# Optimization experiments

Hardware: AMD Instinct MI355X
Metric: run time of the kernel (lower is better)

The kernel has to match this reference:

```python
import math
import jax, jax.numpy as jnp
import numpy as np

B, T, C = 4, 2048, 1024
NH = 16
HD = C // NH  # 64

def setup_inputs() -> dict:
    key = jax.random.key(0)
    k1, k2, k3 = jax.random.split(key, 3)
    x = jax.random.normal(k1, (B, T, C), dtype=jnp.float32)
    # init scale ~ 1/sqrt(fan_in) to keep activations sane
    W_attn = jax.random.normal(k2, (C, 3 * C), dtype=jnp.float32) * (1.0 / math.sqrt(C))
    b_attn = jnp.zeros((3 * C,), dtype=jnp.float32)
    W_proj = jax.random.normal(k3, (C, C), dtype=jnp.float32) * (1.0 / math.sqrt(C))
    b_proj = jnp.zeros((C,), dtype=jnp.float32)
    return {"x": x, "W_attn": W_attn, "b_attn": b_attn, "W_proj": W_proj, "b_proj": b_proj}

def reference(x, W_attn, b_attn, W_proj, b_proj):
    b, t, c = x.shape
    qkv = x @ W_attn + b_attn                      # [B,T,3C]
    q, k, v = jnp.split(qkv, 3, axis=-1)           # each [B,T,C]
    # [B,T,C] -> [B,NH,T,HD]
    def heads(z):
        return z.reshape(b, t, NH, HD).transpose(0, 2, 1, 3)
    q, k, v = heads(q), heads(k), heads(v)
    scale = 1.0 / math.sqrt(HD)
    att = jnp.einsum('bhqd,bhkd->bhqk', q, k) * scale   # [B,NH,T,T]
    causal = jnp.tril(jnp.ones((t, t), dtype=bool))      # [T,T]
    att = jnp.where(causal[None, None, :, :], att, -jnp.inf)
    att = jax.nn.softmax(att, axis=-1)
    # dropout p=0.0 -> identity
    y = jnp.einsum('bhqk,bhkd->bhqd', att, v)            # [B,NH,T,HD]
    y = y.transpose(0, 2, 1, 3).reshape(b, t, c)         # [B,T,C]
    return y @ W_proj + b_proj
```

## Files before the change

kernel.cpp:

```cpp
#include <hip/hip_runtime.h>
#include <hip/hip_bf16.h>


typedef __bf16 bf16;
typedef __bf16 bf16x4 __attribute__((ext_vector_type(4)));
typedef __bf16 bf16x8 __attribute__((ext_vector_type(8)));
typedef float  f32x4  __attribute__((ext_vector_type(4)));

#define MFMA16(a, b, c) __builtin_amdgcn_mfma_f32_16x16x32_bf16((a), (b), (c), 0, 0, 0)

#define GLOAD16(g, l)                                                 \
    __builtin_amdgcn_global_load_lds(                                 \
        (const __attribute__((address_space(1))) void*)(g),           \
        (__attribute__((address_space(3))) void*)(l), 16, 0, 0)

static constexpr int Bsz = 4;
static constexpr int T   = 2048;
static constexpr int Cc  = 1024;
static constexpr int NH  = 16;
static constexpr int HD  = 64;
static constexpr int C3  = 3 * Cc;

__global__ void cvt_f32_bf16(const float* __restrict__ in, bf16* __restrict__ out) {
    size_t i = ((size_t)blockIdx.x * blockDim.x + threadIdx.x) * 8;
    f32x4 a0 = *(const f32x4*)(in + i);
    f32x4 a1 = *(const f32x4*)(in + i + 4);
    bf16x8 v;
#pragma unroll
    for (int e = 0; e < 4; ++e) { v[e] = (bf16)a0[e]; v[e + 4] = (bf16)a1[e]; }
    *(bf16x8*)(out + i) = v;
}

__global__ void transpose_f32_bf16(const float* __restrict__ in, bf16* __restrict__ out,
                                   int R, int Ccols) {
    __shared__ float tile[32][33];
    int bx = blockIdx.x * 32;
    int by = blockIdx.y * 32;
    int tx = threadIdx.x, ty = threadIdx.y;
#pragma unroll
    for (int i = 0; i < 32; i += 8)
        tile[ty + i][tx] = in[(size_t)(by + ty + i) * Ccols + bx + tx];
    __syncthreads();
#pragma unroll
    for (int i = 0; i < 32; i += 8)
        out[(size_t)(bx + ty + i) * R + by + tx] = (bf16)tile[tx][ty + i];
}

__global__ __launch_bounds__(256)
void gemm_qkv(const bf16* __restrict__ A, const bf16* __restrict__ Bt,
              const float* __restrict__ bias,
              bf16* __restrict__ qo, bf16* __restrict__ ko, bf16* __restrict__ vt,
              int M, int N, int K) {
    constexpr int BM = 128, BN = 128, BK = 64;
    __shared__ bf16 As[2][BM * BK];
    __shared__ bf16 Bs[2][BN * BK];

    const int tid  = threadIdx.x;
    const int wave = tid >> 6, lane = tid & 63;
    const int quad = lane >> 4, l16 = lane & 15;
    const int wm = wave & 1, wn = wave >> 1;
    const int m0 = blockIdx.x * BM, n0 = blockIdx.y * BN;

    f32x4 acc[4][4] = {};

    const int lrow = lane >> 3;
    const int lcol = (lane & 7) * 8;
    const bf16* Ab = A  + (size_t)(m0 + wave * 8 + lrow) * K + lcol;
    const bf16* Bb = Bt + (size_t)(n0 + wave * 8 + lrow) * K + lcol;
    const int wofs = wave * 512;

#pragma unroll
    for (int r = 0; r < 4; ++r) {
        GLOAD16(Ab + (size_t)r * 32 * K, As[0] + wofs + r * 2048);
        GLOAD16(Bb + (size_t)r * 32 * K, Bs[0] + wofs + r * 2048);
    }

    int cur = 0;
    for (int k0 = 0; k0 < K; k0 += BK) {
        __syncthreads();
        if (k0 + BK < K) {
#pragma unroll
            for (int r = 0; r < 4; ++r) {
                GLOAD16(Ab + (size_t)r * 32 * K + k0 + BK, As[cur ^ 1] + wofs + r * 2048);
                GLOAD16(Bb + (size_t)r * 32 * K + k0 + BK, Bs[cur ^ 1] + wofs + r * 2048);
            }
        }
        const bf16* Asc = As[cur];
        const bf16* Bsc = Bs[cur];
#pragma unroll
        for (int ks = 0; ks < 2; ++ks) {
            bf16x8 af[4], bfr[4];
#pragma unroll
            for (int i = 0; i < 4; ++i)
                af[i] = *(const bf16x8*)(&Asc[(wm * 64 + i * 16 + l16) * BK + ks * 32 + quad * 8]);
#pragma unroll
            for (int j = 0; j < 4; ++j)
                bfr[j] = *(const bf16x8*)(&Bsc[(wn * 64 + j * 16 + l16) * BK + ks * 32 + quad * 8]);
#pragma unroll
            for (int i = 0; i < 4; ++i)
#pragma unroll
                for (int j = 0; j < 4; ++j)
                    acc[i][j] = MFMA16(af[i], bfr[j], acc[i][j]);
        }
        cur ^= 1;
    }

    const int which = n0 >> 10;
    const int nc0 = n0 & 1023;
    if (which < 2) {
        bf16* dst = which ? ko : qo;
#pragma unroll
        for (int j = 0; j < 4; ++j) {
            int colg = n0 + wn * 64 + j * 16 + l16;
            int coll = nc0 + wn * 64 + j * 16 + l16;
            float bv = bias[colg];
#pragma unroll
            for (int i = 0; i < 4; ++i) {
                int rowb = m0 + wm * 64 + i * 16 + quad * 4;
#pragma unroll
                for (int r = 0; r < 4; ++r)
                    dst[(size_t)(rowb + r) * Cc + coll] = (bf16)(acc[i][j][r] + bv);
            }
        }
    } else {
#pragma unroll
        for (int j = 0; j < 4; ++j) {
            int colg = n0 + wn * 64 + j * 16 + l16;
            int coll = nc0 + wn * 64 + j * 16 + l16;
            int h = coll >> 6, d = coll & 63;
            float bv = bias[colg];
            bf16* vhead_d = vt + ((size_t)h * HD + d) * T;
#pragma unroll
            for (int i = 0; i < 4; ++i) {
                int rowb = m0 + wm * 64 + i * 16 + quad * 4;
                int b = rowb >> 11;
                int t = rowb & 2047;
                bf16x4 pk;
#pragma unroll
                for (int r = 0; r < 4; ++r) pk[r] = (bf16)(acc[i][j][r] + bv);
                *(bf16x4*)(vhead_d + (size_t)b * NH * HD * T + t) = pk;
            }
        }
    }
}

__global__ __launch_bounds__(256)
void gemm_bt(const bf16* __restrict__ A, const bf16* __restrict__ Bt,
             const float* __restrict__ bias, float* __restrict__ C,
             int M, int N, int K) {
    constexpr int BM = 128, BN = 128, BK = 64;
    __shared__ bf16 As[2][BM * BK];
    __shared__ bf16 Bs[2][BN * BK];

    const int tid  = threadIdx.x;
    const int wave = tid >> 6, lane = tid & 63;
    const int quad = lane >> 4, l16 = lane & 15;
    const int wm = wave & 1, wn = wave >> 1;
    const int m0 = blockIdx.x * BM, n0 = blockIdx.y * BN;

    f32x4 acc[4][4] = {};

    const int lrow = lane >> 3;
    const int lcol = (lane & 7) * 8;
    const bf16* Ab = A  + (size_t)(m0 + wave * 8 + lrow) * K + lcol;
    const bf16* Bb = Bt + (size_t)(n0 + wave * 8 + lrow) * K + lcol;
    const int wofs = wave * 512;

#pragma unroll
    for (int r = 0; r < 4; ++r) {
        GLOAD16(Ab + (size_t)r * 32 * K, As[0] + wofs + r * 2048);
        GLOAD16(Bb + (size_t)r * 32 * K, Bs[0] + wofs + r * 2048);
    }

    int cur = 0;
    for (int k0 = 0; k0 < K; k0 += BK) {
        __syncthreads();
        if (k0 + BK < K) {
#pragma unroll
            for (int r = 0; r < 4; ++r) {
                GLOAD16(Ab + (size_t)r * 32 * K + k0 + BK, As[cur ^ 1] + wofs + r * 2048);
                GLOAD16(Bb + (size_t)r * 32 * K + k0 + BK, Bs[cur ^ 1] + wofs + r * 2048);
            }
        }
        const bf16* Asc = As[cur];
        const bf16* Bsc = Bs[cur];
#pragma unroll
        for (int ks = 0; ks < 2; ++ks) {
            bf16x8 af[4], bfr[4];
#pragma unroll
            for (int i = 0; i < 4; ++i)
                af[i] = *(const bf16x8*)(&Asc[(wm * 64 + i * 16 + l16) * BK + ks * 32 + quad * 8]);
#pragma unroll
            for (int j = 0; j < 4; ++j)
                bfr[j] = *(const bf16x8*)(&Bsc[(wn * 64 + j * 16 + l16) * BK + ks * 32 + quad * 8]);
#pragma unroll
            for (int i = 0; i < 4; ++i)
#pragma unroll
                for (int j = 0; j < 4; ++j)
                    acc[i][j] = MFMA16(af[i], bfr[j], acc[i][j]);
        }
        cur ^= 1;
    }

#pragma unroll
    for (int j = 0; j < 4; ++j) {
        int col = n0 + wn * 64 + j * 16 + l16;
        float bv = bias[col];
#pragma unroll
        for (int i = 0; i < 4; ++i) {
            int rowb = m0 + wm * 64 + i * 16 + quad * 4;
#pragma unroll
            for (int r = 0; r < 4; ++r)
                C[(size_t)(rowb + r) * N + col] = acc[i][j][r] + bv;
        }
    }
}

__global__ __launch_bounds__(256)
void attn_fused(const bf16* __restrict__ qb, const bf16* __restrict__ kb,
                const bf16* __restrict__ vtb, bf16* __restrict__ y) {
    constexpr int LKD = 72, LVT = 72, LPS = 72;
    constexpr int QT = T / 128;
    __shared__ bf16 Ks[2][64 * LKD];
    __shared__ bf16 Vt[2][64 * LVT];
    __shared__ bf16 Ps[4][32 * LPS];

    const int tid  = threadIdx.x;
    const int wave = tid >> 6, lane = tid & 63;
    const int quad = lane >> 4, l16 = lane & 15;
    const int bid = blockIdx.x;
    const int pr = bid >> 6;
    const int hb = bid & 63;
    const int b = hb >> 4, h = hb & 15;

    const bf16* qbase  = qb + (size_t)b * T * Cc + h * HD;
    const bf16* kbase  = kb + (size_t)b * T * Cc + h * HD;
    const bf16* vthead = vtb + (size_t)(b * NH + h) * HD * T;
    bf16* yrow = y + (size_t)b * T * Cc + h * HD;

    const int srow = tid >> 2;
    const int sch  = tid & 3;

#pragma unroll 1
    for (int seg = 0; seg < 2; ++seg) {
        const int qt = (seg == 0) ? (QT - 1 - pr) : pr;
        const int q0 = qt * 128;

        bf16x8 qf[2][2];
#pragma unroll
        for (int qn = 0; qn < 2; ++qn) {
            int qrow = q0 + wave * 32 + qn * 16 + l16;
#pragma unroll
            for (int ks = 0; ks < 2; ++ks) {
                bf16x8 v = *(const bf16x8*)(qbase + (size_t)qrow * Cc + ks * 32 + quad * 8);
#pragma unroll
                for (int e = 0; e < 8; ++e) v[e] = (bf16)((float)v[e] * 0.18033688f);
                qf[qn][ks] = v;
            }
        }

        f32x4 o[2][4] = {};
        float lsum[2] = {0.f, 0.f};

        const int w0 = q0 + wave * 32;
        const int nt = q0 / 64 + 2;

        bf16x8 kp[2], vp[2];
#pragma unroll
        for (int c2 = 0; c2 < 2; ++c2) {
            int ch = sch + c2 * 4;
            kp[c2] = *(const bf16x8*)(kbase + (size_t)srow * Cc + ch * 8);
            vp[c2] = *(const bf16x8*)(vthead + (size_t)srow * T + ch * 8);
        }
        __syncthreads();
#pragma unroll
        for (int c2 = 0; c2 < 2; ++c2) {
            int ch = sch + c2 * 4;
            *(bf16x8*)(&Ks[0][srow * LKD + ch * 8]) = kp[c2];
            *(bf16x8*)(&Vt[0][srow * LVT + ch * 8]) = vp[c2];
        }

        int cur = 0;
        for (int it = 0; it < nt; ++it) {
            const int kt = it * 64;
            __syncthreads();

            const bool more = (it + 1 < nt);
            if (more) {
                int ktn = kt + 64;
#pragma unroll
                for (int c2 = 0; c2 < 2; ++c2) {
                    int ch = sch + c2 * 4;
                    kp[c2] = *(const bf16x8*)(kbase + (size_t)(ktn + srow) * Cc + ch * 8);
                    vp[c2] = *(const bf16x8*)(vthead + (size_t)srow * T + ktn + ch * 8);
                }
            }

            const bf16* ksc = Ks[cur];
            const bf16* vtc = Vt[cur];
            if (kt <= w0 + 31) {
                __builtin_amdgcn_s_setprio(1);
                f32x4 st[4][2] = {};
#pragma unroll
                for (int km = 0; km < 4; ++km) {
                    bf16x8 kf0 = *(const bf16x8*)(&ksc[(km * 16 + l16) * LKD + quad * 8]);
                    bf16x8 kf1 = *(const bf16x8*)(&ksc[(km * 16 + l16) * LKD + 32 + quad * 8]);
#pragma unroll
                    for (int qn = 0; qn < 2; ++qn) {
                        st[km][qn] = MFMA16(kf0, qf[qn][0], st[km][qn]);
                        st[km][qn] = MFMA16(kf1, qf[qn][1], st[km][qn]);
                    }
                }

                const bool needmask = (kt + 63 > w0);
                float rs[2] = {0.f, 0.f};
#pragma unroll
                for (int km = 0; km < 4; ++km)
#pragma unroll
                    for (int qn = 0; qn < 2; ++qn) {
                        int qrel = w0 + qn * 16 + l16 - kt;
#pragma unroll
                        for (int r = 0; r < 4; ++r) {
                            float v = st[km][qn][r];
                            if (needmask) {
                                int key = km * 16 + quad * 4 + r;
                                v = (key <= qrel) ? v : -INFINITY;
                            }
                            float p = __builtin_exp2f(v);
                            st[km][qn][r] = p;
                            rs[qn] += p;
                        }
                    }
#pragma unroll
                for (int qn = 0; qn < 2; ++qn) {
                    rs[qn] += __shfl_xor(rs[qn], 16, 64);
                    rs[qn] += __shfl_xor(rs[qn], 32, 64);
                    lsum[qn] += rs[qn];
                }

                bf16* pw = &Ps[wave][0];
#pragma unroll
                for (int qn = 0; qn < 2; ++qn)
#pragma unroll
                    for (int km = 0; km < 4; ++km) {
                        bf16x4 pk;
#pragma unroll
                        for (int r = 0; r < 4; ++r) pk[r] = (bf16)st[km][qn][r];
                        *(bf16x4*)(&pw[(qn * 16 + l16) * LPS + km * 16 + quad * 4]) = pk;
                    }
                bf16x8 pf[2][2];
#pragma unroll
                for (int qn = 0; qn < 2; ++qn)
#pragma unroll
                    for (int ks = 0; ks < 2; ++ks)
                        pf[qn][ks] = *(const bf16x8*)(&pw[(qn * 16 + l16) * LPS + ks * 32 + quad * 8]);

#pragma unroll
                for (int dd = 0; dd < 4; ++dd)
#pragma unroll
                    for (int ks = 0; ks < 2; ++ks) {
                        bf16x8 vf = *(const bf16x8*)(&vtc[(dd * 16 + l16) * LVT + ks * 32 + quad * 8]);
                        o[0][dd] = MFMA16(pf[0][ks], vf, o[0][dd]);
                        o[1][dd] = MFMA16(pf[1][ks], vf, o[1][dd]);
                    }
                __builtin_amdgcn_s_setprio(0);
            }

            if (more) {
#pragma unroll
                for (int c2 = 0; c2 < 2; ++c2) {
                    int ch = sch + c2 * 4;
                    *(bf16x8*)(&Ks[cur ^ 1][srow * LKD + ch * 8]) = kp[c2];
                    *(bf16x8*)(&Vt[cur ^ 1][srow * LVT + ch * 8]) = vp[c2];
                }
            }
            cur ^= 1;
        }

#pragma unroll
        for (int qn = 0; qn < 2; ++qn)
#pragma unroll
            for (int r = 0; r < 4; ++r) {
                float den = __shfl(lsum[qn], (lane & 48) | (quad * 4 + r), 64);
                float inv = 1.0f / den;
                int t = w0 + qn * 16 + quad * 4 + r;
#pragma unroll
                for (int dd = 0; dd < 4; ++dd)
                    yrow[(size_t)t * Cc + dd * 16 + l16] = (bf16)(o[qn][dd][r] * inv);
            }
    }
}

extern "C" void kernel_launch(void* const* d_in, const int* in_sizes, int n_in,
                              void* d_out, int out_size, void* d_ws, size_t ws_size,
                              hipStream_t stream) {
    const float* x      = (const float*)d_in[0];
    const float* W_attn = (const float*)d_in[1];
    const float* b_attn = (const float*)d_in[2];
    const float* W_proj = (const float*)d_in[3];
    const float* b_proj = (const float*)d_in[4];
    float* out = (float*)d_out;

    const int M = Bsz * T;
    const size_t R = (size_t)M * Cc;

    bf16* qb  = (bf16*)d_ws;
    bf16* kb  = qb + R;
    bf16* vtb = kb + R;
    bf16* xb  = vtb + R;
    bf16* yb  = xb;
    bf16* WtA = (bf16*)d_out;
    bf16* WtP = qb;

    dim3 tpb(32, 8);

    cvt_f32_bf16<<<(int)(R / (256 * 8)), 256, 0, stream>>>(x, xb);
    transpose_f32_bf16<<<dim3(C3 / 32, Cc / 32), tpb, 0, stream>>>(W_attn, WtA, Cc, C3);
    gemm_qkv<<<dim3(M / 128, C3 / 128), 256, 0, stream>>>(xb, WtA, b_attn, qb, kb, vtb, M, C3, Cc);
    attn_fused<<<512, 256, 0, stream>>>(qb, kb, vtb, yb);
    transpose_f32_bf16<<<dim3(Cc / 32, Cc / 32), tpb, 0, stream>>>(W_proj, WtP, Cc, Cc);
    gemm_bt<<<dim3(M / 128, Cc / 128), 256, 0, stream>>>(yb, WtP, b_proj, out, M, Cc, Cc);
}
```

Measured before the change: 286.4 us.

## Shrink attention key tile to 32 and compute row sums via MFMA with ones

The attention kernel's key/value tile is halved from 64 to 32 keys per iteration, cutting LDS footprint, and launch bounds now request 4 blocks per CU for higher occupancy. The softmax denominator is no longer accumulated with scalar adds and cross-lane shuffles; an extra MFMA against a vector of ones produces the row sums already in the output layout. This trades twice as many loop iterations and barriers, plus one extra MFMA per tile, for less shuffle work, finer causal skipping and more resident waves.

```diff
diff --git a/kernel.cpp b/kernel.cpp
--- a/kernel.cpp
+++ b/kernel.cpp
@@ -216,12 +216,14 @@
     }
 }
 
-__global__ __launch_bounds__(256)
+__global__ __launch_bounds__(256, 4)
 void attn_fused(const bf16* __restrict__ qb, const bf16* __restrict__ kb,
                 const bf16* __restrict__ vtb, bf16* __restrict__ y) {
-    constexpr int LKD = 72, LVT = 72, LPS = 72;
+    constexpr int LKD = 72;
+    constexpr int LVT = 40;
+    constexpr int LPS = 40;
     constexpr int QT = T / 128;
-    __shared__ bf16 Ks[2][64 * LKD];
+    __shared__ bf16 Ks[2][32 * LKD];
     __shared__ bf16 Vt[2][64 * LVT];
     __shared__ bf16 Ps[4][32 * LPS];
 
@@ -238,8 +240,12 @@
     const bf16* vthead = vtb + (size_t)(b * NH + h) * HD * T;
     bf16* yrow = y + (size_t)b * T * Cc + h * HD;
 
-    const int srow = tid >> 2;
-    const int sch  = tid & 3;
+    const int srK = tid >> 3, scK = (tid & 7) * 8;
+    const int srV = tid >> 2, scV = (tid & 3) * 8;
+
+    bf16x8 ones;
+#pragma unroll
+    for (int e = 0; e < 8; ++e) ones[e] = (bf16)1.0f;
 
 #pragma unroll 1
     for (int seg = 0; seg < 2; ++seg) {
@@ -251,58 +257,45 @@
         for (int qn = 0; qn < 2; ++qn) {
             int qrow = q0 + wave * 32 + qn * 16 + l16;
 #pragma unroll
-            for (int ks = 0; ks < 2; ++ks) {
-                bf16x8 v = *(const bf16x8*)(qbase + (size_t)qrow * Cc + ks * 32 + quad * 8);
+            for (int dblk = 0; dblk < 2; ++dblk) {
+                bf16x8 v = *(const bf16x8*)(qbase + (size_t)qrow * Cc + dblk * 32 + quad * 8);
 #pragma unroll
                 for (int e = 0; e < 8; ++e) v[e] = (bf16)((float)v[e] * 0.18033688f);
-                qf[qn][ks] = v;
+                qf[qn][dblk] = v;
             }
         }
 
         f32x4 o[2][4] = {};
-        float lsum[2] = {0.f, 0.f};
+        f32x4 osum[2] = {};
 
         const int w0 = q0 + wave * 32;
-        const int nt = q0 / 64 + 2;
-
-        bf16x8 kp[2], vp[2];
-#pragma unroll
-        for (int c2 = 0; c2 < 2; ++c2) {
-            int ch = sch + c2 * 4;
-            kp[c2] = *(const bf16x8*)(kbase + (size_t)srow * Cc + ch * 8);
-            vp[c2] = *(const bf16x8*)(vthead + (size_t)srow * T + ch * 8);
-        }
+        const int nt = q0 / 32 + 4;
+
+        bf16x8 kp = *(const bf16x8*)(kbase + (size_t)srK * Cc + scK);
+        bf16x8 vp = *(const bf16x8*)(vthead + (size_t)srV * T + scV);
         __syncthreads();
-#pragma unroll
-        for (int c2 = 0; c2 < 2; ++c2) {
-            int ch = sch + c2 * 4;
-            *(bf16x8*)(&Ks[0][srow * LKD + ch * 8]) = kp[c2];
-            *(bf16x8*)(&Vt[0][srow * LVT + ch * 8]) = vp[c2];
-        }
+        *(bf16x8*)(&Ks[0][srK * LKD + scK]) = kp;
+        *(bf16x8*)(&Vt[0][srV * LVT + scV]) = vp;
 
         int cur = 0;
         for (int it = 0; it < nt; ++it) {
-            const int kt = it * 64;
+            const int kt = it * 32;
             __syncthreads();
 
             const bool more = (it + 1 < nt);
             if (more) {
-                int ktn = kt + 64;
-#pragma unroll
-                for (int c2 = 0; c2 < 2; ++c2) {
-                    int ch = sch + c2 * 4;
-                    kp[c2] = *(const bf16x8*)(kbase + (size_t)(ktn + srow) * Cc + ch * 8);
-                    vp[c2] = *(const bf16x8*)(vthead + (size_t)srow * T + ktn + ch * 8);
-                }
+                int ktn = kt + 32;
+                kp = *(const bf16x8*)(kbase + (size_t)(ktn + srK) * Cc + scK);
+                vp = *(const bf16x8*)(vthead + (size_t)srV * T + ktn + scV);
             }
 
             const bf16* ksc = Ks[cur];
             const bf16* vtc = Vt[cur];
             if (kt <= w0 + 31) {
                 __builtin_amdgcn_s_setprio(1);
-                f32x4 st[4][2] = {};
-#pragma unroll
-                for (int km = 0; km < 4; ++km) {
+                f32x4 st[2][2] = {};
+#pragma unroll
+                for (int km = 0; km < 2; ++km) {
                     bf16x8 kf0 = *(const bf16x8*)(&ksc[(km * 16 + l16) * LKD + quad * 8]);
                     bf16x8 kf1 = *(const bf16x8*)(&ksc[(km * 16 + l16) * LKD + 32 + quad * 8]);
 #pragma unroll
@@ -312,10 +305,9 @@
                     }
                 }
 
-                const bool needmask = (kt + 63 > w0);
-                float rs[2] = {0.f, 0.f};
-#pragma unroll
-                for (int km = 0; km < 4; ++km)
+                const bool needmask = (kt + 31 > w0);
+#pragma unroll
+                for (int km = 0; km < 2; ++km)
 #pragma unroll
                     for (int qn = 0; qn < 2; ++qn) {
                         int qrel = w0 + qn * 16 + l16 - kt;
@@ -326,53 +318,39 @@
                                 int key = km * 16 + quad * 4 + r;
                                 v = (key <= qrel) ? v : -INFINITY;
                             }
-                            float p = __builtin_exp2f(v);
-                            st[km][qn][r] = p;
-                            rs[qn] += p;
+                            st[km][qn][r] = __builtin_exp2f(v);
                         }
                     }
-#pragma unroll
-                for (int qn = 0; qn < 2; ++qn) {
-                    rs[qn] += __shfl_xor(rs[qn], 16, 64);
-                    rs[qn] += __shfl_xor(rs[qn], 32, 64);
-                    lsum[qn] += rs[qn];
-                }
 
                 bf16* pw = &Ps[wave][0];
 #pragma unroll
                 for (int qn = 0; qn < 2; ++qn)
 #pragma unroll
-                    for (int km = 0; km < 4; ++km) {
+                    for (int km = 0; km < 2; ++km) {
                         bf16x4 pk;
 #pragma unroll
                         for (int r = 0; r < 4; ++r) pk[r] = (bf16)st[km][qn][r];
                         *(bf16x4*)(&pw[(qn * 16 + l16) * LPS + km * 16 + quad * 4]) = pk;
                     }
-                bf16x8 pf[2][2];
+                bf16x8 pf[2];
 #pragma unroll
                 for (int qn = 0; qn < 2; ++qn)
-#pragma unroll
-                    for (int ks = 0; ks < 2; ++ks)
-                        pf[qn][ks] = *(const bf16x8*)(&pw[(qn * 16 + l16) * LPS + ks * 32 + quad * 8]);
-
-#pragma unroll
-                for (int dd = 0; dd < 4; ++dd)
-#pragma unroll
-                    for (int ks = 0; ks < 2; ++ks) {
-                        bf16x8 vf = *(const bf16x8*)(&vtc[(dd * 16 + l16) * LVT + ks * 32 + quad * 8]);
-                        o[0][dd] = MFMA16(pf[0][ks], vf, o[0][dd]);
-                        o[1][dd] = MFMA16(pf[1][ks], vf, o[1][dd]);
-                    }
+                    pf[qn] = *(const bf16x8*)(&pw[(qn * 16 + l16) * LPS + quad * 8]);
+
+#pragma unroll
+                for (int dd = 0; dd < 4; ++dd) {
+                    bf16x8 vf = *(const bf16x8*)(&vtc[(dd * 16 + l16) * LVT + quad * 8]);
+                    o[0][dd] = MFMA16(pf[0], vf, o[0][dd]);
+                    o[1][dd] = MFMA16(pf[1], vf, o[1][dd]);
+                }
+                osum[0] = MFMA16(pf[0], ones, osum[0]);
+                osum[1] = MFMA16(pf[1], ones, osum[1]);
                 __builtin_amdgcn_s_setprio(0);
             }
 
             if (more) {
-#pragma unroll
-                for (int c2 = 0; c2 < 2; ++c2) {
-                    int ch = sch + c2 * 4;
-                    *(bf16x8*)(&Ks[cur ^ 1][srow * LKD + ch * 8]) = kp[c2];
-                    *(bf16x8*)(&Vt[cur ^ 1][srow * LVT + ch * 8]) = vp[c2];
-                }
+                *(bf16x8*)(&Ks[cur ^ 1][srK * LKD + scK]) = kp;
+                *(bf16x8*)(&Vt[cur ^ 1][srV * LVT + scV]) = vp;
             }
             cur ^= 1;
         }
@@ -381,8 +359,7 @@
         for (int qn = 0; qn < 2; ++qn)
 #pragma unroll
             for (int r = 0; r < 4; ++r) {
-                float den = __shfl(lsum[qn], (lane & 48) | (quad * 4 + r), 64);
-                float inv = 1.0f / den;
+                float inv = 1.0f / osum[qn][r];
                 int t = w0 + qn * 16 + quad * 4 + r;
 #pragma unroll
                 for (int dd = 0; dd < 4; ++dd)
```

Result: no change. 285.6 us (-0.3%).
